# Kernel optimization log

Measured on AMD Instinct MI355X. Metric: run time of the kernel, lower is better.

## Reference

```python
import jax, jax.numpy as jnp
import numpy as np

H = 128        # hidden_size
V = 100000     # item vocab
B = 1024       # sessions
NODES = 32     # unique nodes per session (sections)
ITEMS = 16     # itemsets per session (sequence_len)
P = 8          # PADDED_LENGTH
N = B * NODES  # total nodes
T = B * ITEMS  # total itemsets


def setup_inputs() -> dict:
    key = jax.random.key(0)
    ks = jax.random.split(key, 10)
    s = 1.0 / np.sqrt(H)
    node_embedding = jax.random.normal(ks[0], (N, H), jnp.float32)
    emb_weight = jax.random.normal(ks[1], (V, H), jnp.float32) * s
    W1_w = jax.random.normal(ks[2], (H, H), jnp.float32) * s
    W1_b = jnp.zeros((H,), jnp.float32)
    W2_w = jax.random.normal(ks[3], (H, H), jnp.float32) * s
    W2_b = jnp.zeros((H,), jnp.float32)
    q_w = jax.random.normal(ks[4], (1, H), jnp.float32) * s
    q_b = jnp.zeros((1,), jnp.float32)
    W3_w = jax.random.normal(ks[5], (H, 2 * H), jnp.float32) * s
    W3_b = jnp.zeros((H,), jnp.float32)
    batch = jnp.repeat(jnp.arange(B, dtype=jnp.int32), NODES)  # sorted segment ids
    # local node indices per itemset; value == NODES means padding (zero row)
    sequence = jax.random.randint(ks[6], (T, P), 0, NODES + 1, jnp.int32)
    sequence = sequence.at[:, 0].set(jnp.minimum(sequence[:, 0], NODES - 1))  # >=1 valid entry
    itemset_len = jnp.sum(sequence < NODES, axis=1).astype(jnp.int32)
    sequence_len = jnp.full((B,), ITEMS, jnp.int32)
    cue = jax.random.randint(ks[7], (B,), 0, V, jnp.int32)
    return dict(node_embedding=node_embedding, emb_weight=emb_weight,
                W1_w=W1_w, W1_b=W1_b, W2_w=W2_w, W2_b=W2_b,
                q_w=q_w, q_b=q_b, W3_w=W3_w, W3_b=W3_b,
                batch=batch, sequence=sequence, itemset_len=itemset_len,
                sequence_len=sequence_len, cue=cue)


def reference(node_embedding, emb_weight, W1_w, W1_b, W2_w, W2_b,
              q_w, q_b, W3_w, W3_b, batch, sequence, itemset_len,
              sequence_len, cue):
    nB = sequence_len.shape[0]
    nN = node_embedding.shape[0]
    nT = sequence.shape[0]
    # per-session node counts (torch.bincount) and exclusive offsets (torch.split)
    sections = jax.ops.segment_sum(jnp.ones_like(batch), batch, num_segments=nB)
    node_off = jnp.cumsum(sections) - sections                      # [B]
    # session id of each itemset (torch.split(sequence, sequence_len))
    seq_cum = jnp.cumsum(sequence_len)                              # [B]
    itemset_seg = jnp.searchsorted(seq_cum, jnp.arange(nT), side='right')  # [T]
    # gather: local index == sections[s] hits the appended zero row -> mask to 0
    sec_t = sections[itemset_seg][:, None]                          # [T,1]
    valid = sequence < sec_t                                        # [T,P]
    gidx = jnp.clip(node_off[itemset_seg][:, None] + sequence, 0, nN - 1)
    gathered = jnp.where(valid[..., None], node_embedding[gidx], 0.0)  # [T,P,H]
    itemset_emb = gathered.sum(axis=1) / itemset_len[:, None].astype(node_embedding.dtype)  # [T,H]
    # last itemset of each session = v_n
    v_n = itemset_emb[seq_cum - 1]                                  # [B,H]
    v_n_rep = v_n[itemset_seg]                                      # [T,H]
    gate = jax.nn.sigmoid(v_n_rep @ W1_w.T + W1_b + itemset_emb @ W2_w.T + W2_b)
    alpha = gate @ q_w.T + q_b                                      # [T,1]
    s_g = jax.ops.segment_sum(alpha * itemset_emb, itemset_seg, num_segments=nB)  # [B,H]
    s_h = jnp.concatenate([v_n, s_g], axis=1) @ W3_w.T + W3_b       # [B,H]
    y_hat = jnp.sum(s_h * emb_weight[cue], axis=1)                  # [B]
    all_scores = s_h @ emb_weight.T                                 # [B,V]
    return (y_hat, all_scores)
```

## Files before the change

### kernel.cpp

```cpp
#include <hip/hip_runtime.h>
#include <hip/hip_bf16.h>

#define H 128
#define VOCAB 100000
#define B_SESS 1024
#define NODES 32
#define ITEMS 16
#define PADLEN 8
#define NCHUNK 32

typedef short short8 __attribute__((ext_vector_type(8)));
typedef float f32x16 __attribute__((ext_vector_type(16)));
typedef float f32x4 __attribute__((ext_vector_type(4)));

static __device__ __forceinline__ short f2bf(float x) {
    unsigned u = __builtin_bit_cast(unsigned, x);
    u += 0x7fffu + ((u >> 16) & 1u);
    return (short)(u >> 16);
}

static __device__ __forceinline__ short8 pack8(f32x4 x, f32x4 y) {
    short8 f;
    f[0] = f2bf(x[0]); f[1] = f2bf(x[1]); f[2] = f2bf(x[2]); f[3] = f2bf(x[3]);
    f[4] = f2bf(y[0]); f[5] = f2bf(y[1]); f[6] = f2bf(y[2]); f[7] = f2bf(y[3]);
    return f;
}

__global__ __launch_bounds__(256) void k_transpose(
    const float* __restrict__ W1, const float* __restrict__ W3,
    float* __restrict__ W1t, float* __restrict__ W3t)
{
    const int idx = blockIdx.x * 256 + threadIdx.x;
    const int k = idx >> 7, j = idx & 127;
    W1t[idx] = W1[j * H + k];
    W3t[k * H + j]       = W3[j * 2 * H + k];
    W3t[(k + H) * H + j] = W3[j * 2 * H + k + H];
}

__global__ __launch_bounds__(H) void k_session(
    const float* __restrict__ node_emb,
    const int* __restrict__ sequence,
    const int* __restrict__ itemset_len,
    const float* __restrict__ W1t, const float* __restrict__ W1_b,
    const float* __restrict__ W2_w, const float* __restrict__ W2_b,
    const float* __restrict__ q_w,  const float* __restrict__ q_b,
    const float* __restrict__ W3t, const float* __restrict__ W3_b,
    const float* __restrict__ emb_weight, const int* __restrict__ cue,
    float* __restrict__ y_hat, short* __restrict__ packA)
{
    __shared__ float it[ITEMS][H];
    __shared__ float pre_lds[H];
    __shared__ float sg[H];
    __shared__ float alphas[ITEMS];
    __shared__ float apart[2][ITEMS];
    __shared__ float wred[2];

    const int b = blockIdx.x;
    const int j = threadIdx.x;
    const int nbase = b * NODES;

#pragma unroll
    for (int t = 0; t < ITEMS; ++t) {
        const int tg = b * ITEMS + t;
        float acc = 0.f;
#pragma unroll
        for (int p = 0; p < PADLEN; ++p) {
            int s = sequence[tg * PADLEN + p];
            if (s < NODES) acc += node_emb[(nbase + s) * H + j];
        }
        it[t][j] = acc / (float)itemset_len[tg];
    }
    __syncthreads();

    {
        float pre = W1_b[j] + W2_b[j];
#pragma unroll 4
        for (int k = 0; k < H; k += 4) {
            float4 v = *(const float4*)&it[ITEMS - 1][k];
            pre += W1t[(k + 0) * H + j] * v.x + W1t[(k + 1) * H + j] * v.y
                 + W1t[(k + 2) * H + j] * v.z + W1t[(k + 3) * H + j] * v.w;
        }
        pre_lds[j] = pre;
    }
    __syncthreads();

    {
        const int w = threadIdx.x >> 6;
        const int l = threadIdx.x & 63;
        const int tA = l & 15, kg = l >> 4;

        short8 afr[4];
#pragma unroll
        for (int s = 0; s < 4; ++s) {
            const f32x4* p = (const f32x4*)&it[tA][s * 32 + kg * 8];
            afr[s] = pack8(p[0], p[1]);
        }

        f32x4 hacc[4];
        float qwc[4];
#pragma unroll
        for (int nt = 0; nt < 4; ++nt) {
            const int jcol = (w * 4 + nt) * 16 + (l & 15);
            qwc[nt] = q_w[jcol];
#pragma unroll
            for (int r = 0; r < 4; ++r) hacc[nt][r] = 0.f;
#pragma unroll
            for (int s = 0; s < 4; ++s) {
                const float* wr = W2_w + jcol * H + s * 32 + kg * 8;
                short8 bfr = pack8(*(const f32x4*)wr, *(const f32x4*)(wr + 4));
                hacc[nt] = __builtin_amdgcn_mfma_f32_16x16x32_bf16(
                    afr[s], bfr, hacc[nt], 0, 0, 0);
            }
        }
#pragma unroll
        for (int r = 0; r < 4; ++r) {
            float s = 0.f;
#pragma unroll
            for (int nt = 0; nt < 4; ++nt) {
                const int jcol = (w * 4 + nt) * 16 + (l & 15);
                float g = 1.f / (1.f + __expf(-(pre_lds[jcol] + hacc[nt][r])));
                s = fmaf(qwc[nt], g, s);
            }
            s += __shfl_xor(s, 1); s += __shfl_xor(s, 2);
            s += __shfl_xor(s, 4); s += __shfl_xor(s, 8);
            if ((l & 15) == 0) apart[w][kg * 4 + r] = s;
        }
    }
    __syncthreads();
    if (threadIdx.x < ITEMS)
        alphas[threadIdx.x] = q_b[0] + apart[0][threadIdx.x] + apart[1][threadIdx.x];
    __syncthreads();

    {
        float sgj = 0.f;
#pragma unroll
        for (int t = 0; t < ITEMS; ++t) sgj = fmaf(alphas[t], it[t][j], sgj);
        sg[j] = sgj;
    }
    __syncthreads();

    float sh = W3_b[j];
#pragma unroll 4
    for (int k = 0; k < H; k += 4) {
        float4 v = *(const float4*)&it[ITEMS - 1][k];
        sh += W3t[(k + 0) * H + j] * v.x + W3t[(k + 1) * H + j] * v.y
            + W3t[(k + 2) * H + j] * v.z + W3t[(k + 3) * H + j] * v.w;
    }
#pragma unroll 4
    for (int k = 0; k < H; k += 4) {
        float4 v = *(const float4*)&sg[k];
        sh += W3t[(H + k + 0) * H + j] * v.x + W3t[(H + k + 1) * H + j] * v.y
            + W3t[(H + k + 2) * H + j] * v.z + W3t[(H + k + 3) * H + j] * v.w;
    }

    {
        const int c = b >> 5, cl = b & 31;
        const int s = j >> 4, hi = (j >> 3) & 1, i = j & 7;
        packA[c * 4096 + s * 512 + hi * 256 + cl * 8 + i] = f2bf(sh);
    }

    float prod = sh * emb_weight[(long)cue[b] * H + j];
#pragma unroll
    for (int off = 32; off > 0; off >>= 1) prod += __shfl_down(prod, off);
    if ((j & 63) == 0) wred[j >> 6] = prod;
    __syncthreads();
    if (j == 0) y_hat[b] = wred[0] + wred[1];
}

__global__ __launch_bounds__(256, 4) void k_scores(
    const float* __restrict__ emb_weight,
    const short* __restrict__ packA,
    float* __restrict__ scores)
{
    const int bid = blockIdx.x;

    const int wave = threadIdx.x >> 6;
    const int lane = threadIdx.x & 63;
    const int hi = lane >> 5;
    const int cl = lane & 31;
    const int col = bid * 128 + wave * 32 + cl;
    const bool valid = col < VOCAB;

    short8 bfrag[8];
    if (valid) {
        const float* row = emb_weight + (long)col * H;
#pragma unroll
        for (int s = 0; s < 8; ++s) {
            const f32x4* p = (const f32x4*)(row + s * 16 + hi * 8);
            bfrag[s] = pack8(p[0], p[1]);
        }
    } else {
#pragma unroll
        for (int s = 0; s < 8; ++s) {
            short8 z;
#pragma unroll
            for (int i = 0; i < 8; ++i) z[i] = 0;
            bfrag[s] = z;
        }
    }

    for (int c = 0; c < NCHUNK; ++c) {
        const short* ap = packA + c * 4096 + hi * 256 + cl * 8;
        short8 a[8];
#pragma unroll
        for (int s = 0; s < 8; ++s) a[s] = *(const short8*)(ap + s * 512);
        f32x16 acc;
#pragma unroll
        for (int r2 = 0; r2 < 16; ++r2) acc[r2] = 0.f;
#pragma unroll
        for (int s = 0; s < 8; ++s)
            acc = __builtin_amdgcn_mfma_f32_32x32x16_bf16(a[s], bfrag[s], acc, 0, 0, 0);
        if (valid) {
            const int M0 = c * 32;
#pragma unroll
            for (int r2 = 0; r2 < 16; ++r2) {
                int rowm = (r2 & 3) + 8 * (r2 >> 2) + 4 * hi;
                __builtin_nontemporal_store(acc[r2],
                    &scores[(long)(M0 + rowm) * VOCAB + col]);
            }
        }
    }
}

extern "C" void kernel_launch(void* const* d_in, const int* in_sizes, int n_in,
                              void* d_out, int out_size, void* d_ws, size_t ws_size,
                              hipStream_t stream) {
    const float* node_emb   = (const float*)d_in[0];
    const float* emb_w      = (const float*)d_in[1];
    const float* W1_w       = (const float*)d_in[2];
    const float* W1_b       = (const float*)d_in[3];
    const float* W2_w       = (const float*)d_in[4];
    const float* W2_b       = (const float*)d_in[5];
    const float* q_w        = (const float*)d_in[6];
    const float* q_b        = (const float*)d_in[7];
    const float* W3_w       = (const float*)d_in[8];
    const float* W3_b       = (const float*)d_in[9];
    const int* sequence     = (const int*)d_in[11];
    const int* itemset_len  = (const int*)d_in[12];
    const int* cue          = (const int*)d_in[14];

    float* out    = (float*)d_out;
    float* y_hat  = out;
    float* scores = out + B_SESS;

    short* packA = (short*)d_ws;
    float* W1t   = (float*)((char*)d_ws + (256 << 10));
    float* W3t   = W1t + H * H;

    k_transpose<<<64, 256, 0, stream>>>(W1_w, W3_w, W1t, W3t);
    k_session<<<B_SESS, H, 0, stream>>>(node_emb, sequence, itemset_len,
                                        W1t, W1_b, W2_w, W2_b,
                                        q_w, q_b, W3t, W3_b, emb_w, cue,
                                        y_hat, packA);
    const int nblk = (VOCAB + 127) / 128;
    k_scores<<<nblk, 256, 0, stream>>>(emb_w, packA, scores);
}
```

Baseline: 135.9 us.

## Fold W1 and W3 matvecs into bf16 MFMA and drop transpose kernel

Moves the W1·v_n projection into the same MFMA K-loop as W2, so the gate pre-activation is computed in one 16x16x32 bf16 accumulation. The W3 projection also uses MFMA, with only row 0 of the A fragment holding data. Weights are now read in their original layout, so the separate transpose kernel and its launch go away. The catch is that the W1 and W3 paths now round to bf16 (lower precision than fp32), and the W3 MFMA spends most of its work on zero rows.

Result: slower. 145.0 us (+6.7%).

```diff
diff --git a/kernel.cpp b/kernel.cpp
--- a/kernel.cpp
+++ b/kernel.cpp
@@ -26,31 +26,20 @@
     return f;
 }
 
-__global__ __launch_bounds__(256) void k_transpose(
-    const float* __restrict__ W1, const float* __restrict__ W3,
-    float* __restrict__ W1t, float* __restrict__ W3t)
-{
-    const int idx = blockIdx.x * 256 + threadIdx.x;
-    const int k = idx >> 7, j = idx & 127;
-    W1t[idx] = W1[j * H + k];
-    W3t[k * H + j]       = W3[j * 2 * H + k];
-    W3t[(k + H) * H + j] = W3[j * 2 * H + k + H];
-}
-
 __global__ __launch_bounds__(H) void k_session(
     const float* __restrict__ node_emb,
     const int* __restrict__ sequence,
     const int* __restrict__ itemset_len,
-    const float* __restrict__ W1t, const float* __restrict__ W1_b,
+    const float* __restrict__ W1_w, const float* __restrict__ W1_b,
     const float* __restrict__ W2_w, const float* __restrict__ W2_b,
     const float* __restrict__ q_w,  const float* __restrict__ q_b,
-    const float* __restrict__ W3t, const float* __restrict__ W3_b,
+    const float* __restrict__ W3_w, const float* __restrict__ W3_b,
     const float* __restrict__ emb_weight, const int* __restrict__ cue,
     float* __restrict__ y_hat, short* __restrict__ packA)
 {
     __shared__ float it[ITEMS][H];
-    __shared__ float pre_lds[H];
     __shared__ float sg[H];
+    __shared__ float sh_lds[H];
     __shared__ float alphas[ITEMS];
     __shared__ float apart[2][ITEMS];
     __shared__ float wred[2];
@@ -72,44 +61,37 @@
     }
     __syncthreads();
 
-    {
-        float pre = W1_b[j] + W2_b[j];
-#pragma unroll 4
-        for (int k = 0; k < H; k += 4) {
-            float4 v = *(const float4*)&it[ITEMS - 1][k];
-            pre += W1t[(k + 0) * H + j] * v.x + W1t[(k + 1) * H + j] * v.y
-                 + W1t[(k + 2) * H + j] * v.z + W1t[(k + 3) * H + j] * v.w;
-        }
-        pre_lds[j] = pre;
-    }
-    __syncthreads();
-
-    {
-        const int w = threadIdx.x >> 6;
-        const int l = threadIdx.x & 63;
-        const int tA = l & 15, kg = l >> 4;
-
-        short8 afr[4];
-#pragma unroll
-        for (int s = 0; s < 4; ++s) {
-            const f32x4* p = (const f32x4*)&it[tA][s * 32 + kg * 8];
-            afr[s] = pack8(p[0], p[1]);
+    const int w = j >> 6;
+    const int l = j & 63;
+    const int tA = l & 15, kg = l >> 4;
+
+    {
+        short8 afrG[8];
+#pragma unroll
+        for (int s = 0; s < 8; ++s) {
+            const float* src = (s < 4) ? &it[tA][s * 32 + kg * 8]
+                                       : &it[ITEMS - 1][(s - 4) * 32 + kg * 8];
+            const f32x4* p = (const f32x4*)src;
+            afrG[s] = pack8(p[0], p[1]);
         }
 
         f32x4 hacc[4];
-        float qwc[4];
+        float qwc[4], b12[4];
 #pragma unroll
         for (int nt = 0; nt < 4; ++nt) {
-            const int jcol = (w * 4 + nt) * 16 + (l & 15);
+            const int jcol = (w * 4 + nt) * 16 + tA;
             qwc[nt] = q_w[jcol];
+            b12[nt] = W1_b[jcol] + W2_b[jcol];
 #pragma unroll
             for (int r = 0; r < 4; ++r) hacc[nt][r] = 0.f;
 #pragma unroll
-            for (int s = 0; s < 4; ++s) {
-                const float* wr = W2_w + jcol * H + s * 32 + kg * 8;
+            for (int s = 0; s < 8; ++s) {
+                const float* wr = (s < 4)
+                    ? (W2_w + jcol * H + s * 32 + kg * 8)
+                    : (W1_w + jcol * H + (s - 4) * 32 + kg * 8);
                 short8 bfr = pack8(*(const f32x4*)wr, *(const f32x4*)(wr + 4));
                 hacc[nt] = __builtin_amdgcn_mfma_f32_16x16x32_bf16(
-                    afr[s], bfr, hacc[nt], 0, 0, 0);
+                    afrG[s], bfr, hacc[nt], 0, 0, 0);
             }
         }
 #pragma unroll
@@ -117,13 +99,12 @@
             float s = 0.f;
 #pragma unroll
             for (int nt = 0; nt < 4; ++nt) {
-                const int jcol = (w * 4 + nt) * 16 + (l & 15);
-                float g = 1.f / (1.f + __expf(-(pre_lds[jcol] + hacc[nt][r])));
+                float g = 1.f / (1.f + __expf(-(b12[nt] + hacc[nt][r])));
                 s = fmaf(qwc[nt], g, s);
             }
             s += __shfl_xor(s, 1); s += __shfl_xor(s, 2);
             s += __shfl_xor(s, 4); s += __shfl_xor(s, 8);
-            if ((l & 15) == 0) apart[w][kg * 4 + r] = s;
+            if (tA == 0) apart[w][kg * 4 + r] = s;
         }
     }
     __syncthreads();
@@ -139,19 +120,42 @@
     }
     __syncthreads();
 
-    float sh = W3_b[j];
-#pragma unroll 4
-    for (int k = 0; k < H; k += 4) {
-        float4 v = *(const float4*)&it[ITEMS - 1][k];
-        sh += W3t[(k + 0) * H + j] * v.x + W3t[(k + 1) * H + j] * v.y
-            + W3t[(k + 2) * H + j] * v.z + W3t[(k + 3) * H + j] * v.w;
-    }
-#pragma unroll 4
-    for (int k = 0; k < H; k += 4) {
-        float4 v = *(const float4*)&sg[k];
-        sh += W3t[(H + k + 0) * H + j] * v.x + W3t[(H + k + 1) * H + j] * v.y
-            + W3t[(H + k + 2) * H + j] * v.z + W3t[(H + k + 3) * H + j] * v.w;
-    }
+    {
+        short8 afrS[8];
+#pragma unroll
+        for (int s = 0; s < 8; ++s) {
+            if (tA == 0) {
+                const float* src = (s < 4) ? &it[ITEMS - 1][s * 32 + kg * 8]
+                                           : &sg[(s - 4) * 32 + kg * 8];
+                const f32x4* p = (const f32x4*)src;
+                afrS[s] = pack8(p[0], p[1]);
+            } else {
+                short8 z;
+#pragma unroll
+                for (int i = 0; i < 8; ++i) z[i] = 0;
+                afrS[s] = z;
+            }
+        }
+#pragma unroll
+        for (int nt = 0; nt < 4; ++nt) {
+            const int jcol = (w * 4 + nt) * 16 + tA;
+            f32x4 sacc;
+#pragma unroll
+            for (int r = 0; r < 4; ++r) sacc[r] = 0.f;
+            const float* wr0 = W3_w + jcol * (2 * H);
+#pragma unroll
+            for (int s = 0; s < 8; ++s) {
+                const float* wr = wr0 + s * 32 + kg * 8;
+                short8 bfr = pack8(*(const f32x4*)wr, *(const f32x4*)(wr + 4));
+                sacc = __builtin_amdgcn_mfma_f32_16x16x32_bf16(
+                    afrS[s], bfr, sacc, 0, 0, 0);
+            }
+            if (kg == 0) sh_lds[jcol] = W3_b[jcol] + sacc[0];
+        }
+    }
+    __syncthreads();
+
+    const float sh = sh_lds[j];
 
     {
         const int c = b >> 5, cl = b & 31;
@@ -244,13 +248,10 @@
     float* scores = out + B_SESS;
 
     short* packA = (short*)d_ws;
-    float* W1t   = (float*)((char*)d_ws + (256 << 10));
-    float* W3t   = W1t + H * H;
-
-    k_transpose<<<64, 256, 0, stream>>>(W1_w, W3_w, W1t, W3t);
+
     k_session<<<B_SESS, H, 0, stream>>>(node_emb, sequence, itemset_len,
-                                        W1t, W1_b, W2_w, W2_b,
-                                        q_w, q_b, W3t, W3_b, emb_w, cue,
+                                        W1_w, W1_b, W2_w, W2_b,
+                                        q_w, q_b, W3_w, W3_b, emb_w, cue,
                                         y_hat, packA);
     const int nblk = (VOCAB + 127) / 128;
     k_scores<<<nblk, 256, 0, stream>>>(emb_w, packA, scores);
```
